# Performance work log

Hardware: AMD Instinct MI355X
Metric: run time of the kernel (lower is better)

## Reference

```python
import jax, jax.numpy as jnp
import numpy as np

B, T, C, NH = 8, 512, 512, 8
HD = C // NH

def _layernorm(x, g, b, eps=1e-5):
    mu = jnp.mean(x, axis=-1, keepdims=True)
    var = jnp.var(x, axis=-1, keepdims=True)
    return (x - mu) * jax.lax.rsqrt(var + eps) * g + b

def setup_inputs() -> dict:
    key = jax.random.key(0)
    ks = jax.random.split(key, 5)
    return {
        "x": jax.random.normal(ks[0], (B, T, C), jnp.float32),
        "w_attn": jax.random.normal(ks[1], (3 * C, C), jnp.float32) * (1.0 / np.sqrt(C)),
        "b_attn": jnp.zeros((3 * C,), jnp.float32),
        "w_proj": jax.random.normal(ks[2], (C, C), jnp.float32) * (1.0 / np.sqrt(C)),
        "b_proj": jnp.zeros((C,), jnp.float32),
        "q_gamma": jnp.ones((C,), jnp.float32),
        "q_beta": jnp.zeros((C,), jnp.float32),
        "k_gamma": jnp.ones((C,), jnp.float32),
        "k_beta": jnp.zeros((C,), jnp.float32),
        "rel_emb": jax.random.normal(ks[3], (T, C), jnp.float32) * 0.02,
    }

def reference(x, w_attn, b_attn, w_proj, b_proj, q_gamma, q_beta, k_gamma, k_beta, rel_emb):
    b, t, c = x.shape
    # QKV projection (torch Linear: x @ W.T + b)
    qkv = x @ w_attn.T + b_attn                       # [B,T,3C]
    q, k, v = jnp.split(qkv, 3, axis=-1)
    # per-stream LayerNorm over full embedding dim (q_ln/k_ln = LayerNorm(n_embd))
    q = _layernorm(q, q_gamma, q_beta)
    k = _layernorm(k, k_gamma, k_beta)
    # split heads -> [B,NH,T,HD]
    q = q.reshape(b, t, NH, HD).transpose(0, 2, 1, 3)
    k = k.reshape(b, t, NH, HD).transpose(0, 2, 1, 3)
    v = v.reshape(b, t, NH, HD).transpose(0, 2, 1, 3)
    # relative-position bias: gather rel_emb[|i-j|] -> [T,T,NH,HD]
    idx = jnp.abs(jnp.arange(t)[None, :] - jnp.arange(t)[:, None])  # [T,T] int
    rel = rel_emb[idx].reshape(t, t, NH, HD)
    rel_bias = jnp.einsum("bhqd,qkhd->bhqk", q, rel)  # [B,NH,T,T]
    scale = 1.0 / np.sqrt(HD)
    scores = (jnp.einsum("bhqd,bhkd->bhqk", q, k) + rel_bias) * scale
    causal = jnp.tril(jnp.ones((t, t), bool))
    scores = jnp.where(causal[None, None], scores, jnp.finfo(scores.dtype).min)
    att = jax.nn.softmax(scores, axis=-1)
    y = jnp.einsum("bhqk,bhkd->bhqd", att, v)         # [B,NH,T,HD]
    y = y.transpose(0, 2, 1, 3).reshape(b, t, c)
    return y @ w_proj.T + b_proj
```

## Files before the change

### kernel.cpp

```cpp
#include <hip/hip_runtime.h>
#include <hip/hip_bf16.h>
#include <cstddef>

#define BB 8
#define TT 512
#define CC 512
#define NHH 8
#define HDD 64

typedef __attribute__((ext_vector_type(8))) short short8;
typedef __attribute__((ext_vector_type(4))) float f32x4;

__device__ __forceinline__ unsigned short f2bf(float f) {
    unsigned u = __float_as_uint(f);
    u += 0x7FFFu + ((u >> 16) & 1u);
    return (unsigned short)(u >> 16);
}
__device__ __forceinline__ float bf2f(unsigned short h) {
    return __uint_as_float(((unsigned)h) << 16);
}

__global__ __launch_bounds__(256) void cvt_all_k(
    const float* __restrict__ x, const float* __restrict__ wa,
    const float* __restrict__ wp, const float* __restrict__ rel,
    unsigned short* __restrict__ Xb, unsigned short* __restrict__ Wqb,
    unsigned short* __restrict__ Wpb, unsigned short* __restrict__ Relb)
{
    const int bidx = blockIdx.x;
    const float* in;
    unsigned short* out;
    int base;
    if (bidx < 2048)      { in = x;   out = Xb;   base = bidx; }
    else if (bidx < 2816) { in = wa;  out = Wqb;  base = bidx - 2048; }
    else if (bidx < 3072) { in = wp;  out = Wpb;  base = bidx - 2816; }
    else                  { in = rel; out = Relb; base = bidx - 3072; }
    const int i = base * 1024 + threadIdx.x * 4;
    const float4 v = *(const float4*)(in + i);
    unsigned short tmp[4] = {f2bf(v.x), f2bf(v.y), f2bf(v.z), f2bf(v.w)};
    *(uint2*)(out + i) = *(const uint2*)tmp;
}

__global__ __launch_bounds__(256, 2) void gemm_qkv_mfma(
    const unsigned short* __restrict__ Xb, const unsigned short* __restrict__ Wb,
    const float* __restrict__ bias, unsigned short* __restrict__ qkbuf,
    unsigned short* __restrict__ VT)
{
    __shared__ __align__(16) unsigned short lds[128 * 136];

    const int tid = threadIdx.x;
    const int w = tid >> 6, lane = tid & 63;
    const int c = lane & 15, quad = lane >> 4;
    const int wm = w >> 1, wn = w & 1;
    const int bm = blockIdx.y * 128, bn = blockIdx.x * 128;

    const unsigned short* pp[8];
#pragma unroll
    for (int l = 0; l < 8; ++l) {
        const int ci = w * 8 + l;
        if (ci < 16) {
            const int m16 = ci >> 1, kk = ci & 1;
            pp[l] = Xb + (size_t)(bm + m16 * 16 + c) * 512 + kk * 32 + quad * 8;
        } else {
            const int cb = ci - 16, n16 = cb >> 1, kk = cb & 1;
            pp[l] = Wb + (size_t)(bn + n16 * 16 + c) * 512 + kk * 32 + quad * 8;
        }
    }

    f32x4 acc[4][4];
#pragma unroll
    for (int i = 0; i < 4; ++i)
#pragma unroll
        for (int j = 0; j < 4; ++j) acc[i][j] = (f32x4){0.f, 0.f, 0.f, 0.f};

    short8 pre[8];
#pragma unroll
    for (int l = 0; l < 8; ++l) pre[l] = *(const short8*)pp[l];

    for (int k0 = 0; k0 < 512; k0 += 64) {
        __syncthreads();
#pragma unroll
        for (int l = 0; l < 8; ++l)
            *(short8*)&lds[(w * 8 + l) * 512 + lane * 8] = pre[l];
        __syncthreads();
        if (k0 + 64 < 512) {
#pragma unroll
            for (int l = 0; l < 8; ++l)
                pre[l] = *(const short8*)(pp[l] + k0 + 64);
        }
#pragma unroll
        for (int kk = 0; kk < 2; ++kk) {
            short8 af[4], bfr[4];
#pragma unroll
            for (int i = 0; i < 4; ++i)
                af[i] = *(const short8*)&lds[((wm * 4 + i) * 2 + kk) * 512 + lane * 8];
#pragma unroll
            for (int j = 0; j < 4; ++j)
                bfr[j] = *(const short8*)&lds[(16 + (wn * 4 + j) * 2 + kk) * 512 + lane * 8];
#pragma unroll
            for (int i = 0; i < 4; ++i)
#pragma unroll
                for (int j = 0; j < 4; ++j)
                    acc[i][j] = __builtin_amdgcn_mfma_f32_16x16x32_bf16(
                        af[i], bfr[j], acc[i][j], 0, 0, 0);
        }
    }

    float bj[4];
#pragma unroll
    for (int j = 0; j < 4; ++j) bj[j] = bias[bn + wn * 64 + j * 16 + c];

    if (bn < 1024) {
#pragma unroll
        for (int i = 0; i < 4; ++i)
#pragma unroll
            for (int j = 0; j < 4; ++j) {
                const int n = bn + wn * 64 + j * 16 + c;
#pragma unroll
                for (int r = 0; r < 4; ++r) {
                    const int m = bm + wm * 64 + i * 16 + quad * 4 + r;
                    qkbuf[(size_t)m * 1024 + n] = f2bf(acc[i][j][r] + bj[j]);
                }
            }
    } else {
        __syncthreads();
#pragma unroll
        for (int i = 0; i < 4; ++i)
#pragma unroll
            for (int j = 0; j < 4; ++j) {
                const int col = wn * 64 + j * 16 + c;
                const int row0 = wm * 64 + i * 16 + quad * 4;
                unsigned short t4[4];
#pragma unroll
                for (int r = 0; r < 4; ++r) t4[r] = f2bf(acc[i][j][r] + bj[j]);
                *(uint2*)&lds[col * 136 + row0] = *(const uint2*)t4;
            }
        __syncthreads();
        const int bi = bm >> 9, tb = bm & 511;
        const int hd0 = bn - 1024;
#pragma unroll
        for (int l = 0; l < 8; ++l) {
            const int idx = l * 256 + tid;
            const int col = idx >> 4, grp = idx & 15;
            const short8 v = *(const short8*)&lds[col * 136 + grp * 8];
            const int hd = hd0 + col, h = hd >> 6, d = hd & 63;
            *(short8*)(VT + ((size_t)(bi * NHH + h) * HDD + d) * TT + tb + grp * 8) = v;
        }
    }
}

__global__ __launch_bounds__(256) void ln_k(
    const unsigned short* __restrict__ qkbuf,
    const float* __restrict__ qg, const float* __restrict__ qb,
    const float* __restrict__ kg, const float* __restrict__ kb,
    unsigned short* __restrict__ Qh, unsigned short* __restrict__ Kh)
{
    const int wv = threadIdx.x >> 6, lane = threadIdx.x & 63;
    const int row = blockIdx.x * 4 + wv;
    const int bi = row >> 9, t = row & 511;
    const unsigned short* base = qkbuf + (size_t)row * 1024;

#pragma unroll
    for (int s = 0; s < 2; ++s) {
        const short8 v8 = *(const short8*)(base + s * 512 + lane * 8);
        float vf[8];
#pragma unroll
        for (int i = 0; i < 8; ++i) vf[i] = bf2f(((const unsigned short*)&v8)[i]);
        float sum = 0.f, sq = 0.f;
#pragma unroll
        for (int i = 0; i < 8; ++i) { sum += vf[i]; sq += vf[i] * vf[i]; }
#pragma unroll
        for (int off = 1; off < 64; off <<= 1) {
            sum += __shfl_xor(sum, off);
            sq += __shfl_xor(sq, off);
        }
        const float mu = sum * (1.f / 512.f);
        const float var = sq * (1.f / 512.f) - mu * mu;
        const float rsg = rsqrtf(var + 1e-5f);
        const float* gam = (s ? kg : qg) + lane * 8;
        const float* bet = (s ? kb : qb) + lane * 8;
        const float4 g0 = *(const float4*)gam, g1 = *(const float4*)(gam + 4);
        const float4 b0 = *(const float4*)bet, b1 = *(const float4*)(bet + 4);
        const float gv[8] = {g0.x, g0.y, g0.z, g0.w, g1.x, g1.y, g1.z, g1.w};
        const float bv[8] = {b0.x, b0.y, b0.z, b0.w, b1.x, b1.y, b1.z, b1.w};
        unsigned short o8[8];
#pragma unroll
        for (int i = 0; i < 8; ++i)
            o8[i] = f2bf((vf[i] - mu) * rsg * gv[i] + bv[i]);
        unsigned short* outp = s ? Kh : Qh;
        *(short8*)(outp + ((size_t)(bi * NHH + (lane >> 3)) * TT + t) * HDD
                   + (lane & 7) * 8) = *(const short8*)o8;
    }
}

#define RD_DIRECT(nr_, mb_)                                                     \
    {                                                                           \
        int mrow = (mb_) + (nr_) * 16 + c;                                      \
        mrow = mrow < 0 ? 0 : (mrow > 511 ? 511 : mrow);                        \
        const unsigned short* gp = Rbase + (size_t)mrow * CC + quad * 8;        \
        const short8 br0 = *(const short8*)gp;                                  \
        const short8 br1 = *(const short8*)(gp + 32);                           \
        f32x4 a2 = (f32x4){0.f, 0.f, 0.f, 0.f};                                 \
        a2 = __builtin_amdgcn_mfma_f32_16x16x32_bf16(aq0, br0, a2, 0, 0, 0);    \
        a2 = __builtin_amdgcn_mfma_f32_16x16x32_bf16(aq1, br1, a2, 0, 0, 0);    \
        const int colw = ((mb_) + (nr_) * 16 + c) & 127;                        \
        _Pragma("unroll")                                                       \
        for (int r = 0; r < 4; ++r)                                             \
            RDs[w][(quad * 4 + r) * 132 + colw] = f2bf(a2[r]);                  \
    }

__global__ __launch_bounds__(256, 2) void attn_k(
    const unsigned short* __restrict__ Qh, const unsigned short* __restrict__ Kh,
    const unsigned short* __restrict__ VT, const unsigned short* __restrict__ Relb,
    unsigned short* __restrict__ Yb)
{
    __shared__ __align__(16) unsigned short Ps[4][16 * 72];
    __shared__ __align__(16) unsigned short RDs[4][16 * 132];

    const int tid = threadIdx.x;
    const int w = tid >> 6;
    const int lane = tid & 63;
    const int c = lane & 15;
    const int quad = lane >> 4;

    const int bid = blockIdx.x;
    const int bit0 = bid & 1, bit8 = (bid >> 8) & 1;
    const int s_ = bit0 ^ bit8;
    const int q0 = (bid >> 1) & 7;
    const int qt = s_ ? 7 - q0 : q0;
    const int h = (bid >> 4) & 7;
    const int b = ((bid >> 7) & 1) | (bit8 << 1) | (bit0 << 2);
    const int i0 = qt * 64;

    const unsigned short* Qbase = Qh + (size_t)(b * NHH + h) * TT * HDD;
    const unsigned short* Kbase = Kh + (size_t)(b * NHH + h) * TT * HDD;
    const unsigned short* Vbase = VT + (size_t)(b * NHH + h) * HDD * TT;
    const unsigned short* Rbase = Relb + h * HDD;

    const unsigned short* qp = Qbase + (size_t)(i0 + w * 16 + c) * HDD + quad * 8;
    const short8 aq0 = *(const short8*)qp;
    const short8 aq1 = *(const short8*)(qp + 32);

    f32x4 oacc[4];
    float m_i[4], l_i[4];
#pragma unroll
    for (int r = 0; r < 4; ++r) { m_i[r] = -1e30f; l_i[r] = 0.f; }
#pragma unroll
    for (int nd = 0; nd < 4; ++nd) oacc[nd] = (f32x4){0.f, 0.f, 0.f, 0.f};

    {
        const int mb0 = i0 - 63;
#pragma unroll
        for (int nr = 4; nr < 8; ++nr) RD_DIRECT(nr, mb0)
    }

    for (int jt = 0; jt <= qt; ++jt) {
        const int j0 = jt * 64;
        const int mbase = i0 - j0 - 63;

        short8 bk0[4], bk1[4], bv0[4], bv1[4];
#pragma unroll
        for (int ns = 0; ns < 4; ++ns) {
            const unsigned short* kp =
                Kbase + (size_t)(j0 + ns * 16 + c) * HDD + quad * 8;
            bk0[ns] = *(const short8*)kp;
            bk1[ns] = *(const short8*)(kp + 32);
        }
#pragma unroll
        for (int nd = 0; nd < 4; ++nd) {
            const unsigned short* vp =
                Vbase + (size_t)(nd * 16 + c) * TT + j0 + quad * 8;
            bv0[nd] = *(const short8*)vp;
            bv1[nd] = *(const short8*)(vp + 32);
        }

#pragma unroll
        for (int nr = 0; nr < 4; ++nr) RD_DIRECT(nr, mbase)

        f32x4 sAcc[4];
#pragma unroll
        for (int ns = 0; ns < 4; ++ns) {
            f32x4 a2 = (f32x4){0.f, 0.f, 0.f, 0.f};
            a2 = __builtin_amdgcn_mfma_f32_16x16x32_bf16(aq0, bk0[ns], a2, 0, 0, 0);
            a2 = __builtin_amdgcn_mfma_f32_16x16x32_bf16(aq1, bk1[ns], a2, 0, 0, 0);
            sAcc[ns] = a2;
        }

        const int dbase = i0 - j0;
        float sc[4][4];
#pragma unroll
        for (int ns = 0; ns < 4; ++ns) {
#pragma unroll
            for (int r = 0; r < 4; ++r) {
                const int r16 = quad * 4 + r;
                const int jc = ns * 16 + c;
                const int dp = (dbase + w * 16 + r16 - jc) & 127;
                const float rdv = bf2f(RDs[w][r16 * 132 + dp]);
                const float v = (sAcc[ns][r] + rdv) * 0.125f;
                sc[ns][r] = (j0 + jc > i0 + w * 16 + r16) ? -1e30f : v;
            }
        }
        float alpha[4];
#pragma unroll
        for (int r = 0; r < 4; ++r) {
            float m = fmaxf(fmaxf(sc[0][r], sc[1][r]), fmaxf(sc[2][r], sc[3][r]));
#pragma unroll
            for (int off = 1; off < 16; off <<= 1) m = fmaxf(m, __shfl_xor(m, off));
            const float mn = fmaxf(m_i[r], m);
            alpha[r] = __expf(m_i[r] - mn);
            m_i[r] = mn;
        }
        float rs[4] = {0.f, 0.f, 0.f, 0.f};
#pragma unroll
        for (int ns = 0; ns < 4; ++ns) {
#pragma unroll
            for (int r = 0; r < 4; ++r) {
                const float p = __expf(sc[ns][r] - m_i[r]);
                rs[r] += p;
                Ps[w][(quad * 4 + r) * 72 + ns * 16 + c] = f2bf(p);
            }
        }
#pragma unroll
        for (int r = 0; r < 4; ++r) {
#pragma unroll
            for (int off = 1; off < 16; off <<= 1) rs[r] += __shfl_xor(rs[r], off);
            l_i[r] = l_i[r] * alpha[r] + rs[r];
        }
#pragma unroll
        for (int nd = 0; nd < 4; ++nd)
#pragma unroll
            for (int r = 0; r < 4; ++r) oacc[nd][r] *= alpha[r];

        const short8 ap0 = *(const short8*)&Ps[w][c * 72 + 0 * 32 + quad * 8];
        const short8 ap1 = *(const short8*)&Ps[w][c * 72 + 1 * 32 + quad * 8];
#pragma unroll
        for (int nd = 0; nd < 4; ++nd) {
            oacc[nd] = __builtin_amdgcn_mfma_f32_16x16x32_bf16(ap0, bv0[nd], oacc[nd], 0, 0, 0);
            oacc[nd] = __builtin_amdgcn_mfma_f32_16x16x32_bf16(ap1, bv1[nd], oacc[nd], 0, 0, 0);
        }
    }

#pragma unroll
    for (int r = 0; r < 4; ++r) {
        const float inv = 1.f / l_i[r];
        const int trow = i0 + w * 16 + quad * 4 + r;
        unsigned short* yb = Yb + ((size_t)b * TT + trow) * CC + h * HDD;
#pragma unroll
        for (int nd = 0; nd < 4; ++nd)
            yb[nd * 16 + c] = f2bf(oacc[nd][r] * inv);
    }
}

__global__ __launch_bounds__(256, 2) void gemm_proj_mfma(
    const unsigned short* __restrict__ Yb, const unsigned short* __restrict__ Wp,
    const float* __restrict__ bias, float* __restrict__ out)
{
    __shared__ __align__(16) unsigned short lds[24 * 512];

    const int tid = threadIdx.x;
    const int w = tid >> 6, lane = tid & 63;
    const int c = lane & 15, quad = lane >> 4;
    const int wm = w >> 1, wn = w & 1;
    const int bm = blockIdx.y * 64, bn = blockIdx.x * 128;

    const unsigned short* pp[6];
#pragma unroll
    for (int l = 0; l < 6; ++l) {
        const int ci = w * 6 + l;
        if (ci < 8) {
            const int m16 = ci >> 1, kk = ci & 1;
            pp[l] = Yb + (size_t)(bm + m16 * 16 + c) * 512 + kk * 32 + quad * 8;
        } else {
            const int cb = ci - 8, n16 = cb >> 1, kk = cb & 1;
            pp[l] = Wp + (size_t)(bn + n16 * 16 + c) * 512 + kk * 32 + quad * 8;
        }
    }

    f32x4 acc[2][4];
#pragma unroll
    for (int i = 0; i < 2; ++i)
#pragma unroll
        for (int j = 0; j < 4; ++j) acc[i][j] = (f32x4){0.f, 0.f, 0.f, 0.f};

    short8 pre[6];
#pragma unroll
    for (int l = 0; l < 6; ++l) pre[l] = *(const short8*)pp[l];

    for (int k0 = 0; k0 < 512; k0 += 64) {
        __syncthreads();
#pragma unroll
        for (int l = 0; l < 6; ++l)
            *(short8*)&lds[(w * 6 + l) * 512 + lane * 8] = pre[l];
        __syncthreads();
        if (k0 + 64 < 512) {
#pragma unroll
            for (int l = 0; l < 6; ++l)
                pre[l] = *(const short8*)(pp[l] + k0 + 64);
        }
#pragma unroll
        for (int kk = 0; kk < 2; ++kk) {
            short8 af[2], bfr[4];
#pragma unroll
            for (int i = 0; i < 2; ++i)
                af[i] = *(const short8*)&lds[((wm * 2 + i) * 2 + kk) * 512 + lane * 8];
#pragma unroll
            for (int j = 0; j < 4; ++j)
                bfr[j] = *(const short8*)&lds[(8 + (wn * 4 + j) * 2 + kk) * 512 + lane * 8];
#pragma unroll
            for (int i = 0; i < 2; ++i)
#pragma unroll
                for (int j = 0; j < 4; ++j)
                    acc[i][j] = __builtin_amdgcn_mfma_f32_16x16x32_bf16(
                        af[i], bfr[j], acc[i][j], 0, 0, 0);
        }
    }

#pragma unroll
    for (int j = 0; j < 4; ++j) {
        const int n = bn + wn * 64 + j * 16 + c;
        const float bj = bias[n];
#pragma unroll
        for (int i = 0; i < 2; ++i)
#pragma unroll
            for (int r = 0; r < 4; ++r) {
                const int m = bm + wm * 32 + i * 16 + quad * 4 + r;
                out[(size_t)m * 512 + n] = acc[i][j][r] + bj;
            }
    }
}

extern "C" void kernel_launch(void* const* d_in, const int* in_sizes, int n_in,
                              void* d_out, int out_size, void* d_ws, size_t ws_size,
                              hipStream_t stream)
{
    const float* x      = (const float*)d_in[0];
    const float* w_attn = (const float*)d_in[1];
    const float* b_attn = (const float*)d_in[2];
    const float* w_proj = (const float*)d_in[3];
    const float* b_proj = (const float*)d_in[4];
    const float* q_g    = (const float*)d_in[5];
    const float* q_b    = (const float*)d_in[6];
    const float* k_g    = (const float*)d_in[7];
    const float* k_b    = (const float*)d_in[8];
    const float* rel    = (const float*)d_in[9];
    float* out = (float*)d_out;

    unsigned short* qkbuf = (unsigned short*)d_ws;
    unsigned short* Qh   = qkbuf + (size_t)4096 * 1024;
    unsigned short* Kh   = Qh + (size_t)4096 * 512;
    unsigned short* VT   = Kh + (size_t)4096 * 512;
    unsigned short* Relb = VT + (size_t)4096 * 512;
    unsigned short* Xb   = Relb + (size_t)512 * 512;
    unsigned short* Wqb  = Xb + (size_t)4096 * 512;
    unsigned short* Wpb  = Wqb + (size_t)1536 * 512;
    unsigned short* Yb   = qkbuf;

    cvt_all_k<<<3328, 256, 0, stream>>>(x, w_attn, w_proj, rel, Xb, Wqb, Wpb, Relb);
    gemm_qkv_mfma<<<dim3(12, 32), 256, 0, stream>>>(Xb, Wqb, b_attn, qkbuf, VT);
    ln_k<<<1024, 256, 0, stream>>>(qkbuf, q_g, q_b, k_g, k_b, Qh, Kh);
    attn_k<<<512, 256, 0, stream>>>(Qh, Kh, VT, Relb, Yb);
    gemm_proj_mfma<<<dim3(4, 64), 256, 0, stream>>>(Yb, Wpb, b_proj, out);
}
```

Baseline: 142.9 us.

## Split attention KV range across two blocks and merge partials in a new kernel

Each query tile's causal key range is split into two halves handled by separate blocks, doubling the grid to improve load balance and occupancy. Each block writes unnormalized fp32 partial outputs plus row max and sum, and a new merge kernel combines them with log-sum-exp weights into the bf16 Y buffer. The occupancy hint is raised to 3 blocks per SM. This trades extra fp32 global traffic and an additional launch for more parallelism on the long causal rows.

```diff
diff --git a/kernel.cpp b/kernel.cpp
--- a/kernel.cpp
+++ b/kernel.cpp
@@ -208,10 +208,10 @@
             RDs[w][(quad * 4 + r) * 132 + colw] = f2bf(a2[r]);                  \
     }
 
-__global__ __launch_bounds__(256, 2) void attn_k(
+__global__ __launch_bounds__(256, 3) void attn_k(
     const unsigned short* __restrict__ Qh, const unsigned short* __restrict__ Kh,
     const unsigned short* __restrict__ VT, const unsigned short* __restrict__ Relb,
-    unsigned short* __restrict__ Yb)
+    float* __restrict__ Opart, float* __restrict__ ML)
 {
     __shared__ __align__(16) unsigned short Ps[4][16 * 72];
     __shared__ __align__(16) unsigned short RDs[4][16 * 132];
@@ -223,13 +223,20 @@
     const int quad = lane >> 4;
 
     const int bid = blockIdx.x;
-    const int bit0 = bid & 1, bit8 = (bid >> 8) & 1;
+    const int half = bid >> 9;
+    const int r9 = bid & 511;
+    const int bit0 = r9 & 1, bit8 = (r9 >> 8) & 1;
     const int s_ = bit0 ^ bit8;
-    const int q0 = (bid >> 1) & 7;
+    const int q0 = (r9 >> 1) & 7;
     const int qt = s_ ? 7 - q0 : q0;
-    const int h = (bid >> 4) & 7;
-    const int b = ((bid >> 7) & 1) | (bit8 << 1) | (bit0 << 2);
+    const int h = (r9 >> 4) & 7;
+    const int b = ((r9 >> 7) & 1) | (bit8 << 1) | (bit0 << 2);
     const int i0 = qt * 64;
+
+    const int jt_mid = (qt + 2) >> 1;
+    const int jt_lo = half ? jt_mid : 0;
+    const int jt_hi = half ? qt + 1 : jt_mid;
+    if (jt_lo >= jt_hi) return;
 
     const unsigned short* Qbase = Qh + (size_t)(b * NHH + h) * TT * HDD;
     const unsigned short* Kbase = Kh + (size_t)(b * NHH + h) * TT * HDD;
@@ -248,12 +255,12 @@
     for (int nd = 0; nd < 4; ++nd) oacc[nd] = (f32x4){0.f, 0.f, 0.f, 0.f};
 
     {
-        const int mb0 = i0 - 63;
+        const int mb0 = i0 - jt_lo * 64 - 63;
 #pragma unroll
         for (int nr = 4; nr < 8; ++nr) RD_DIRECT(nr, mb0)
     }
 
-    for (int jt = 0; jt <= qt; ++jt) {
+    for (int jt = jt_lo; jt < jt_hi; ++jt) {
         const int j0 = jt * 64;
         const int mbase = i0 - j0 - 63;
 
@@ -341,13 +348,62 @@
 
 #pragma unroll
     for (int r = 0; r < 4; ++r) {
-        const float inv = 1.f / l_i[r];
         const int trow = i0 + w * 16 + quad * 4 + r;
-        unsigned short* yb = Yb + ((size_t)b * TT + trow) * CC + h * HDD;
+        float* ob = Opart + (((size_t)(half * BB + b) * TT + trow) * NHH + h) * HDD;
 #pragma unroll
         for (int nd = 0; nd < 4; ++nd)
-            yb[nd * 16 + c] = f2bf(oacc[nd][r] * inv);
-    }
+            ob[nd * 16 + c] = oacc[nd][r];
+        if (c == 0) {
+            float* mlp = ML + (((size_t)half * 64 + b * 8 + h) * TT + trow) * 2;
+            mlp[0] = m_i[r];
+            mlp[1] = l_i[r];
+        }
+    }
+}
+
+__global__ __launch_bounds__(256) void merge_k(
+    const float* __restrict__ Opart, const float* __restrict__ ML,
+    unsigned short* __restrict__ Yb)
+{
+    const int wv = threadIdx.x >> 6, lane = threadIdx.x & 63;
+    const int row = blockIdx.x * 4 + wv;
+    const int b = row >> 9, t = row & 511;
+    const int qt = t >> 6;
+    const int h = lane >> 3, d0 = (lane & 7) * 8;
+
+    const float* mlp0 = ML + (((size_t)0 * 64 + b * 8 + h) * TT + t) * 2;
+    const float m0 = mlp0[0], l0 = mlp0[1];
+    const float* o0p = Opart + (((size_t)(0 * BB + b) * TT + t) * NHH + h) * HDD + d0;
+    float4 oa0 = *(const float4*)o0p;
+    float4 ob0 = *(const float4*)(o0p + 4);
+
+    float o[8];
+    if (qt > 0) {
+        const float* mlp1 = ML + (((size_t)1 * 64 + b * 8 + h) * TT + t) * 2;
+        const float m1 = mlp1[0], l1 = mlp1[1];
+        const float* o1p = Opart + (((size_t)(1 * BB + b) * TT + t) * NHH + h) * HDD + d0;
+        const float4 oa1 = *(const float4*)o1p;
+        const float4 ob1 = *(const float4*)(o1p + 4);
+        const float m = fmaxf(m0, m1);
+        const float w0 = __expf(m0 - m), w1 = __expf(m1 - m);
+        const float inv = 1.f / (l0 * w0 + l1 * w1);
+        o[0] = (oa0.x * w0 + oa1.x * w1) * inv;
+        o[1] = (oa0.y * w0 + oa1.y * w1) * inv;
+        o[2] = (oa0.z * w0 + oa1.z * w1) * inv;
+        o[3] = (oa0.w * w0 + oa1.w * w1) * inv;
+        o[4] = (ob0.x * w0 + ob1.x * w1) * inv;
+        o[5] = (ob0.y * w0 + ob1.y * w1) * inv;
+        o[6] = (ob0.z * w0 + ob1.z * w1) * inv;
+        o[7] = (ob0.w * w0 + ob1.w * w1) * inv;
+    } else {
+        const float inv = 1.f / l0;
+        o[0] = oa0.x * inv; o[1] = oa0.y * inv; o[2] = oa0.z * inv; o[3] = oa0.w * inv;
+        o[4] = ob0.x * inv; o[5] = ob0.y * inv; o[6] = ob0.z * inv; o[7] = ob0.w * inv;
+    }
+    unsigned short o8[8];
+#pragma unroll
+    for (int i = 0; i < 8; ++i) o8[i] = f2bf(o[i]);
+    *(short8*)(Yb + ((size_t)(b * TT + t)) * CC + h * HDD + d0) = *(const short8*)o8;
 }
 
 __global__ __launch_bounds__(256, 2) void gemm_proj_mfma(
@@ -452,11 +508,14 @@
     unsigned short* Xb   = Relb + (size_t)512 * 512;
     unsigned short* Wqb  = Xb + (size_t)4096 * 512;
     unsigned short* Wpb  = Wqb + (size_t)1536 * 512;
-    unsigned short* Yb   = qkbuf;
+    float* Opart = (float*)(Wpb + (size_t)512 * 512);
+    float* ML    = Opart + (size_t)2 * BB * TT * NHH * HDD;
+    unsigned short* Yb = qkbuf;
 
     cvt_all_k<<<3328, 256, 0, stream>>>(x, w_attn, w_proj, rel, Xb, Wqb, Wpb, Relb);
     gemm_qkv_mfma<<<dim3(12, 32), 256, 0, stream>>>(Xb, Wqb, b_attn, qkbuf, VT);
     ln_k<<<1024, 256, 0, stream>>>(qkbuf, q_g, q_b, k_g, k_b, Qh, Kh);
-    attn_k<<<512, 256, 0, stream>>>(Qh, Kh, VT, Relb, Yb);
+    attn_k<<<1024, 256, 0, stream>>>(Qh, Kh, VT, Relb, Opart, ML);
+    merge_k<<<1024, 256, 0, stream>>>(Opart, ML, Yb);
     gemm_proj_mfma<<<dim3(4, 64), 256, 0, stream>>>(Yb, Wpb, b_proj, out);
 }
```

Result: slower. 157.2 us (+10.0%).

## Widen attention key tiles to 128 with causal skipping; shrink QKV GEMM M-tile

Applied to the files above, without the earlier changes.

The attention kernel now walks keys in 128-wide tiles instead of 64, computing relative-position products for 8 row groups per step. It skips score and PV MFMAs for key sub-blocks that lie fully beyond the causal limit. K and V fragments are loaded inside the compute loop rather than prefetched up front, which reduces live registers but exposes load latency. Separately, the QKV GEMM uses 64-row tiles with a doubled grid and a launch bound of 3 blocks per CU, aiming for more parallelism and occupancy at the cost of less reuse per block.

```diff
diff --git a/kernel.cpp b/kernel.cpp
--- a/kernel.cpp
+++ b/kernel.cpp
@@ -40,64 +40,64 @@
     *(uint2*)(out + i) = *(const uint2*)tmp;
 }
 
-__global__ __launch_bounds__(256, 2) void gemm_qkv_mfma(
+__global__ __launch_bounds__(256, 3) void gemm_qkv_mfma(
     const unsigned short* __restrict__ Xb, const unsigned short* __restrict__ Wb,
     const float* __restrict__ bias, unsigned short* __restrict__ qkbuf,
     unsigned short* __restrict__ VT)
 {
-    __shared__ __align__(16) unsigned short lds[128 * 136];
+    __shared__ __align__(16) unsigned short lds[24 * 512];
 
     const int tid = threadIdx.x;
     const int w = tid >> 6, lane = tid & 63;
     const int c = lane & 15, quad = lane >> 4;
     const int wm = w >> 1, wn = w & 1;
-    const int bm = blockIdx.y * 128, bn = blockIdx.x * 128;
-
-    const unsigned short* pp[8];
-#pragma unroll
-    for (int l = 0; l < 8; ++l) {
-        const int ci = w * 8 + l;
-        if (ci < 16) {
+    const int bm = blockIdx.y * 64, bn = blockIdx.x * 128;
+
+    const unsigned short* pp[6];
+#pragma unroll
+    for (int l = 0; l < 6; ++l) {
+        const int ci = w * 6 + l;
+        if (ci < 8) {
             const int m16 = ci >> 1, kk = ci & 1;
             pp[l] = Xb + (size_t)(bm + m16 * 16 + c) * 512 + kk * 32 + quad * 8;
         } else {
-            const int cb = ci - 16, n16 = cb >> 1, kk = cb & 1;
+            const int cb = ci - 8, n16 = cb >> 1, kk = cb & 1;
             pp[l] = Wb + (size_t)(bn + n16 * 16 + c) * 512 + kk * 32 + quad * 8;
         }
     }
 
-    f32x4 acc[4][4];
-#pragma unroll
-    for (int i = 0; i < 4; ++i)
+    f32x4 acc[2][4];
+#pragma unroll
+    for (int i = 0; i < 2; ++i)
 #pragma unroll
         for (int j = 0; j < 4; ++j) acc[i][j] = (f32x4){0.f, 0.f, 0.f, 0.f};
 
-    short8 pre[8];
-#pragma unroll
-    for (int l = 0; l < 8; ++l) pre[l] = *(const short8*)pp[l];
+    short8 pre[6];
+#pragma unroll
+    for (int l = 0; l < 6; ++l) pre[l] = *(const short8*)pp[l];
 
     for (int k0 = 0; k0 < 512; k0 += 64) {
         __syncthreads();
 #pragma unroll
-        for (int l = 0; l < 8; ++l)
-            *(short8*)&lds[(w * 8 + l) * 512 + lane * 8] = pre[l];
+        for (int l = 0; l < 6; ++l)
+            *(short8*)&lds[(w * 6 + l) * 512 + lane * 8] = pre[l];
         __syncthreads();
         if (k0 + 64 < 512) {
 #pragma unroll
-            for (int l = 0; l < 8; ++l)
+            for (int l = 0; l < 6; ++l)
                 pre[l] = *(const short8*)(pp[l] + k0 + 64);
         }
 #pragma unroll
         for (int kk = 0; kk < 2; ++kk) {
-            short8 af[4], bfr[4];
-#pragma unroll
-            for (int i = 0; i < 4; ++i)
-                af[i] = *(const short8*)&lds[((wm * 4 + i) * 2 + kk) * 512 + lane * 8];
+            short8 af[2], bfr[4];
+#pragma unroll
+            for (int i = 0; i < 2; ++i)
+                af[i] = *(const short8*)&lds[((wm * 2 + i) * 2 + kk) * 512 + lane * 8];
 #pragma unroll
             for (int j = 0; j < 4; ++j)
-                bfr[j] = *(const short8*)&lds[(16 + (wn * 4 + j) * 2 + kk) * 512 + lane * 8];
-#pragma unroll
-            for (int i = 0; i < 4; ++i)
+                bfr[j] = *(const short8*)&lds[(8 + (wn * 4 + j) * 2 + kk) * 512 + lane * 8];
+#pragma unroll
+            for (int i = 0; i < 2; ++i)
 #pragma unroll
                 for (int j = 0; j < 4; ++j)
                     acc[i][j] = __builtin_amdgcn_mfma_f32_16x16x32_bf16(
@@ -111,37 +111,37 @@
 
     if (bn < 1024) {
 #pragma unroll
-        for (int i = 0; i < 4; ++i)
+        for (int i = 0; i < 2; ++i)
 #pragma unroll
             for (int j = 0; j < 4; ++j) {
                 const int n = bn + wn * 64 + j * 16 + c;
 #pragma unroll
                 for (int r = 0; r < 4; ++r) {
-                    const int m = bm + wm * 64 + i * 16 + quad * 4 + r;
+                    const int m = bm + wm * 32 + i * 16 + quad * 4 + r;
                     qkbuf[(size_t)m * 1024 + n] = f2bf(acc[i][j][r] + bj[j]);
                 }
             }
     } else {
         __syncthreads();
 #pragma unroll
-        for (int i = 0; i < 4; ++i)
+        for (int i = 0; i < 2; ++i)
 #pragma unroll
             for (int j = 0; j < 4; ++j) {
                 const int col = wn * 64 + j * 16 + c;
-                const int row0 = wm * 64 + i * 16 + quad * 4;
+                const int row0 = wm * 32 + i * 16 + quad * 4;
                 unsigned short t4[4];
 #pragma unroll
                 for (int r = 0; r < 4; ++r) t4[r] = f2bf(acc[i][j][r] + bj[j]);
-                *(uint2*)&lds[col * 136 + row0] = *(const uint2*)t4;
+                *(uint2*)&lds[col * 72 + row0] = *(const uint2*)t4;
             }
         __syncthreads();
         const int bi = bm >> 9, tb = bm & 511;
         const int hd0 = bn - 1024;
 #pragma unroll
-        for (int l = 0; l < 8; ++l) {
+        for (int l = 0; l < 4; ++l) {
             const int idx = l * 256 + tid;
-            const int col = idx >> 4, grp = idx & 15;
-            const short8 v = *(const short8*)&lds[col * 136 + grp * 8];
+            const int col = idx >> 3, grp = idx & 7;
+            const short8 v = *(const short8*)&lds[col * 72 + grp * 8];
             const int hd = hd0 + col, h = hd >> 6, d = hd & 63;
             *(short8*)(VT + ((size_t)(bi * NHH + h) * HDD + d) * TT + tb + grp * 8) = v;
         }
@@ -202,10 +202,10 @@
         f32x4 a2 = (f32x4){0.f, 0.f, 0.f, 0.f};                                 \
         a2 = __builtin_amdgcn_mfma_f32_16x16x32_bf16(aq0, br0, a2, 0, 0, 0);    \
         a2 = __builtin_amdgcn_mfma_f32_16x16x32_bf16(aq1, br1, a2, 0, 0, 0);    \
-        const int colw = ((mb_) + (nr_) * 16 + c) & 127;                        \
+        const int colw = ((mb_) + (nr_) * 16 + c) & 255;                        \
         _Pragma("unroll")                                                       \
         for (int r = 0; r < 4; ++r)                                             \
-            RDs[w][(quad * 4 + r) * 132 + colw] = f2bf(a2[r]);                  \
+            RDs[w][(quad * 4 + r) * 260 + colw] = f2bf(a2[r]);                  \
     }
 
 __global__ __launch_bounds__(256, 2) void attn_k(
@@ -213,8 +213,8 @@
     const unsigned short* __restrict__ VT, const unsigned short* __restrict__ Relb,
     unsigned short* __restrict__ Yb)
 {
-    __shared__ __align__(16) unsigned short Ps[4][16 * 72];
-    __shared__ __align__(16) unsigned short RDs[4][16 * 132];
+    __shared__ __align__(16) unsigned short Ps[4][16 * 136];
+    __shared__ __align__(16) unsigned short RDs[4][16 * 260];
 
     const int tid = threadIdx.x;
     const int w = tid >> 6;
@@ -231,12 +231,12 @@
     const int b = ((bid >> 7) & 1) | (bit8 << 1) | (bit0 << 2);
     const int i0 = qt * 64;
 
-    const unsigned short* Qbase = Qh + (size_t)(b * NHH + h) * TT * HDD;
     const unsigned short* Kbase = Kh + (size_t)(b * NHH + h) * TT * HDD;
     const unsigned short* Vbase = VT + (size_t)(b * NHH + h) * HDD * TT;
     const unsigned short* Rbase = Relb + h * HDD;
 
-    const unsigned short* qp = Qbase + (size_t)(i0 + w * 16 + c) * HDD + quad * 8;
+    const unsigned short* qp = Qh + (size_t)(b * NHH + h) * TT * HDD
+                               + (size_t)(i0 + w * 16 + c) * HDD + quad * 8;
     const short8 aq0 = *(const short8*)qp;
     const short8 aq1 = *(const short8*)(qp + 32);
 
@@ -248,61 +248,53 @@
     for (int nd = 0; nd < 4; ++nd) oacc[nd] = (f32x4){0.f, 0.f, 0.f, 0.f};
 
     {
-        const int mb0 = i0 - 63;
-#pragma unroll
-        for (int nr = 4; nr < 8; ++nr) RD_DIRECT(nr, mb0)
-    }
-
-    for (int jt = 0; jt <= qt; ++jt) {
-        const int j0 = jt * 64;
-        const int mbase = i0 - j0 - 63;
-
-        short8 bk0[4], bk1[4], bv0[4], bv1[4];
-#pragma unroll
-        for (int ns = 0; ns < 4; ++ns) {
-            const unsigned short* kp =
-                Kbase + (size_t)(j0 + ns * 16 + c) * HDD + quad * 8;
-            bk0[ns] = *(const short8*)kp;
-            bk1[ns] = *(const short8*)(kp + 32);
-        }
-#pragma unroll
-        for (int nd = 0; nd < 4; ++nd) {
-            const unsigned short* vp =
-                Vbase + (size_t)(nd * 16 + c) * TT + j0 + quad * 8;
-            bv0[nd] = *(const short8*)vp;
-            bv1[nd] = *(const short8*)(vp + 32);
-        }
-
-#pragma unroll
-        for (int nr = 0; nr < 4; ++nr) RD_DIRECT(nr, mbase)
-
-        f32x4 sAcc[4];
-#pragma unroll
-        for (int ns = 0; ns < 4; ++ns) {
-            f32x4 a2 = (f32x4){0.f, 0.f, 0.f, 0.f};
-            a2 = __builtin_amdgcn_mfma_f32_16x16x32_bf16(aq0, bk0[ns], a2, 0, 0, 0);
-            a2 = __builtin_amdgcn_mfma_f32_16x16x32_bf16(aq1, bk1[ns], a2, 0, 0, 0);
-            sAcc[ns] = a2;
-        }
+        const int mb0 = i0 + 1;
+#pragma unroll
+        for (int nr = 0; nr < 4; ++nr) RD_DIRECT(nr, mb0)
+    }
+
+    const int nIter = (qt + 2) >> 1;
+    for (int it = 0; it < nIter; ++it) {
+        const int j0 = it * 128;
+        const int lim = i0 + 63 - j0;
+        const int nsM = (lim >> 4) >= 7 ? 8 : (lim >> 4) + 1;
+        const int kkM = (lim >> 5) >= 3 ? 4 : (lim >> 5) + 1;
+        const int mbase = i0 - j0 - 127;
+
+#pragma unroll
+        for (int nr = 0; nr < 8; ++nr) RD_DIRECT(nr, mbase)
 
         const int dbase = i0 - j0;
-        float sc[4][4];
-#pragma unroll
-        for (int ns = 0; ns < 4; ++ns) {
-#pragma unroll
-            for (int r = 0; r < 4; ++r) {
-                const int r16 = quad * 4 + r;
+        float sc[8][4];
+#pragma unroll
+        for (int ns = 0; ns < 8; ++ns) {
+            if (ns < nsM) {
+                const unsigned short* kp =
+                    Kbase + (size_t)(j0 + ns * 16 + c) * HDD + quad * 8;
+                const short8 bk0 = *(const short8*)kp;
+                const short8 bk1 = *(const short8*)(kp + 32);
+                f32x4 a2 = (f32x4){0.f, 0.f, 0.f, 0.f};
+                a2 = __builtin_amdgcn_mfma_f32_16x16x32_bf16(aq0, bk0, a2, 0, 0, 0);
+                a2 = __builtin_amdgcn_mfma_f32_16x16x32_bf16(aq1, bk1, a2, 0, 0, 0);
                 const int jc = ns * 16 + c;
-                const int dp = (dbase + w * 16 + r16 - jc) & 127;
-                const float rdv = bf2f(RDs[w][r16 * 132 + dp]);
-                const float v = (sAcc[ns][r] + rdv) * 0.125f;
-                sc[ns][r] = (j0 + jc > i0 + w * 16 + r16) ? -1e30f : v;
-            }
-        }
+#pragma unroll
+                for (int r = 0; r < 4; ++r) {
+                    const int r16 = quad * 4 + r;
+                    const int dp = (dbase + w * 16 + r16 - jc) & 255;
+                    const float rdv = bf2f(RDs[w][r16 * 260 + dp]);
+                    const float v = (a2[r] + rdv) * 0.125f;
+                    sc[ns][r] = (j0 + jc > i0 + w * 16 + r16) ? -1e30f : v;
+                }
+            }
+        }
+
         float alpha[4];
 #pragma unroll
         for (int r = 0; r < 4; ++r) {
-            float m = fmaxf(fmaxf(sc[0][r], sc[1][r]), fmaxf(sc[2][r], sc[3][r]));
+            float m = -1e30f;
+#pragma unroll
+            for (int ns = 0; ns < 8; ++ns)
+                if (ns < nsM) m = fmaxf(m, sc[ns][r]);
 #pragma unroll
             for (int off = 1; off < 16; off <<= 1) m = fmaxf(m, __shfl_xor(m, off));
             const float mn = fmaxf(m_i[r], m);
@@ -311,12 +303,16 @@
         }
         float rs[4] = {0.f, 0.f, 0.f, 0.f};
 #pragma unroll
-        for (int ns = 0; ns < 4; ++ns) {
+        for (int ns = 0; ns < 8; ++ns) {
 #pragma unroll
             for (int r = 0; r < 4; ++r) {
-                const float p = __expf(sc[ns][r] - m_i[r]);
-                rs[r] += p;
-                Ps[w][(quad * 4 + r) * 72 + ns * 16 + c] = f2bf(p);
+                unsigned short pv = 0;
+                if (ns < nsM) {
+                    const float p = __expf(sc[ns][r] - m_i[r]);
+                    rs[r] += p;
+                    pv = f2bf(p);
+                }
+                Ps[w][(quad * 4 + r) * 136 + ns * 16 + c] = pv;
             }
         }
 #pragma unroll
@@ -330,12 +326,20 @@
 #pragma unroll
             for (int r = 0; r < 4; ++r) oacc[nd][r] *= alpha[r];
 
-        const short8 ap0 = *(const short8*)&Ps[w][c * 72 + 0 * 32 + quad * 8];
-        const short8 ap1 = *(const short8*)&Ps[w][c * 72 + 1 * 32 + quad * 8];
-#pragma unroll
-        for (int nd = 0; nd < 4; ++nd) {
-            oacc[nd] = __builtin_amdgcn_mfma_f32_16x16x32_bf16(ap0, bv0[nd], oacc[nd], 0, 0, 0);
-            oacc[nd] = __builtin_amdgcn_mfma_f32_16x16x32_bf16(ap1, bv1[nd], oacc[nd], 0, 0, 0);
+#pragma unroll
+        for (int kk = 0; kk < 4; ++kk) {
+            if (kk < kkM) {
+                const short8 ap =
+                    *(const short8*)&Ps[w][c * 136 + kk * 32 + quad * 8];
+#pragma unroll
+                for (int nd = 0; nd < 4; ++nd) {
+                    const unsigned short* vp =
+                        Vbase + (size_t)(nd * 16 + c) * TT + j0 + kk * 32 + quad * 8;
+                    const short8 bv = *(const short8*)vp;
+                    oacc[nd] = __builtin_amdgcn_mfma_f32_16x16x32_bf16(
+                        ap, bv, oacc[nd], 0, 0, 0);
+                }
+            }
         }
     }
 
@@ -455,7 +459,7 @@
     unsigned short* Yb   = qkbuf;
 
     cvt_all_k<<<3328, 256, 0, stream>>>(x, w_attn, w_proj, rel, Xb, Wqb, Wpb, Relb);
-    gemm_qkv_mfma<<<dim3(12, 32), 256, 0, stream>>>(Xb, Wqb, b_attn, qkbuf, VT);
+    gemm_qkv_mfma<<<dim3(12, 64), 256, 0, stream>>>(Xb, Wqb, b_attn, qkbuf, VT);
     ln_k<<<1024, 256, 0, stream>>>(qkbuf, q_g, q_b, k_g, k_b, Qh, Kh);
     attn_k<<<512, 256, 0, stream>>>(Qh, Kh, VT, Relb, Yb);
     gemm_proj_mfma<<<dim3(4, 64), 256, 0, stream>>>(Yb, Wpb, b_proj, out);
```

Measured after the change: 155.4 us. 8.7% more time.
